# Kernel tuning notes

Measured on AMD Instinct MI355X. Metric: run time of the kernel, lower is better.

## Reference

```python
import jax, jax.numpy as jnp
import numpy as np

B, IMG, P, D, E, S, K, L = 2, 512, 16, 384, 768, 16, 4, 12
G = IMG // P
N = G * G  # 1024 patches

def layer_norm(x, w, b):
    m = x.mean(-1, keepdims=True)
    v = ((x - m) ** 2).mean(-1, keepdims=True)
    return (x - m) / jnp.sqrt(v + 1e-5) * w + b

def silu(x):
    return x * jax.nn.sigmoid(x)

def patch_embed(px, w, b, pos):
    Bz = px.shape[0]
    # non-overlapping patchify == stride-P conv with PxP kernel
    x = px.reshape(Bz, 3, G, P, G, P).transpose(0, 2, 4, 1, 3, 5).reshape(Bz, N, 3 * P * P)
    return x @ w.reshape(D, -1).T + b + pos

def mamba_block(x, norm_w, norm_b, in_w, in_b, conv_w, conv_b, xp_w, xp_b, dt_w, dt_b, A, Dp, out_w, out_b):
    res = x
    x = layer_norm(x, norm_w, norm_b)
    xz = x @ in_w.T + in_b                       # (B,N,2E)
    x_main, z = jnp.split(xz, 2, axis=-1)
    # depthwise causal conv (torch pads K-1 both sides then truncates to N == left pad K-1)
    xc = jax.lax.conv_general_dilated(x_main.transpose(0, 2, 1), conv_w, (1,), [(K - 1, 0)],
                                      dimension_numbers=('NCH', 'OIH', 'NCH'), feature_group_count=E)
    xc = silu((xc + conv_b[:, None]).transpose(0, 2, 1))  # (B,N,E)
    xBC = xc @ xp_w.T + xp_b
    xB, xC = jnp.split(xBC, 2, axis=-1)          # each (B,N,S)
    dt = jnp.clip(jax.nn.softplus(xB @ dt_w.T + dt_b), 1e-4, 1.0)    # (B,N,E)
    dA = jnp.exp(jnp.clip(dt[..., None] * A[None, None], -20.0, 0.0))  # (B,N,E,S)

    def step(h, inp):
        dA_i, xB_i, xC_i, xc_i = inp             # (B,E,S),(B,S),(B,S),(B,E)
        h = dA_i * h + xB_i[:, None, :] * xc_i[:, :, None]
        return h, jnp.einsum('bes,bs->be', h, xC_i)

    h0 = jnp.zeros((x.shape[0], E, S), x.dtype)
    _, ys = jax.lax.scan(step, h0, (dA.transpose(1, 0, 2, 3), xB.transpose(1, 0, 2),
                                    xC.transpose(1, 0, 2), xc.transpose(1, 0, 2)))
    y = ys.transpose(1, 0, 2)                    # (B,N,E)
    y = (y + Dp * xc) * silu(z)
    return res + y @ out_w.T + out_b

def setup_inputs() -> dict:
    key = jax.random.key(0)
    ks = jax.random.split(key, 10)
    rnd = lambda k, shape, s=0.02: jax.random.normal(k, shape, jnp.float32) * s
    return {
        'pixel_values': jax.random.normal(ks[0], (B, 3, IMG, IMG), jnp.float32),
        'patch_w': rnd(ks[1], (D, 3, P, P)),
        'patch_b': jnp.zeros((D,), jnp.float32),
        'pos_embed': rnd(ks[2], (1, N, D)),
        'norm_w': jnp.ones((L, D), jnp.float32), 'norm_b': jnp.zeros((L, D), jnp.float32),
        'in_w': rnd(ks[3], (L, 2 * E, D)), 'in_b': jnp.zeros((L, 2 * E), jnp.float32),
        'conv_w': rnd(ks[4], (L, E, 1, K), 0.3), 'conv_b': jnp.zeros((L, E), jnp.float32),
        'xp_w': rnd(ks[5], (L, 2 * S, E)), 'xp_b': jnp.zeros((L, 2 * S), jnp.float32),
        'dt_w': rnd(ks[6], (L, E, S), 0.1), 'dt_b': jnp.zeros((L, E), jnp.float32),
        'A': -jnp.tile(jnp.arange(1, S + 1, dtype=jnp.float32), (L, E, 1)),
        'Dp': jnp.ones((L, E), jnp.float32),
        'out_w': rnd(ks[7], (L, D, E)), 'out_b': jnp.zeros((L, D), jnp.float32),
        'fnorm_w': jnp.ones((D,), jnp.float32), 'fnorm_b': jnp.zeros((D,), jnp.float32),
        'scale_w': rnd(ks[8], (3, D, D)), 'scale_b': jnp.zeros((3, D), jnp.float32),
    }

def reference(pixel_values, patch_w, patch_b, pos_embed, norm_w, norm_b, in_w, in_b,
              conv_w, conv_b, xp_w, xp_b, dt_w, dt_b, A, Dp, out_w, out_b,
              fnorm_w, fnorm_b, scale_w, scale_b):
    x = patch_embed(pixel_values, patch_w, patch_b, pos_embed)
    layers_per_scale = L // 3
    scales = []
    for i in range(L):
        x = mamba_block(x, norm_w[i], norm_b[i], in_w[i], in_b[i], conv_w[i], conv_b[i],
                        xp_w[i], xp_b[i], dt_w[i], dt_b[i], A[i], Dp[i], out_w[i], out_b[i])
        if i % layers_per_scale == 0 and i // layers_per_scale < 3:
            j = i // layers_per_scale
            scales.append(x @ scale_w[j].T + scale_b[j])
    feats = layer_norm(x, fnorm_w, fnorm_b)
    # stacked: [features, scale_4, scale_8, scale_16] -> (4, B, N, D)
    return jnp.stack([feats] + scales)
```

## Files before the change

### kernel.cpp

```cpp
#include <hip/hip_runtime.h>
#include <hip/hip_bf16.h>

constexpr int Bz = 2, IMG = 512, Pp = 16, D = 384, E = 768, S = 16, L = 12;
constexpr int G = IMG / Pp;
constexpr int Np = G * G;
constexpr int M = Bz * Np;
constexpr int TWO_E = 2 * E;

typedef short bf16x8 __attribute__((ext_vector_type(8)));
typedef float fx4    __attribute__((ext_vector_type(4)));

static __device__ __forceinline__ unsigned short f2bf(float f){
  unsigned int u = __float_as_uint(f);
  u = (u + 0x7FFFu + ((u >> 16) & 1u)) >> 16;
  return (unsigned short)u;
}
static __device__ __forceinline__ float bf2f(unsigned short h){
  return __uint_as_float(((unsigned int)h) << 16);
}

template<int N>
static __device__ __forceinline__ float ror_add(float v){
  int x = __builtin_amdgcn_update_dpp(0, __float_as_int(v), 0x120 | N, 0xF, 0xF, true);
  return v + __int_as_float(x);
}
static __device__ __forceinline__ float row_sum16(float v){
  v = ror_add<8>(v); v = ror_add<4>(v); v = ror_add<2>(v); v = ror_add<1>(v);
  return v;
}

constexpr size_t PW_N = (size_t)D * 768;
constexpr size_t IW_N = (size_t)L * TWO_E * D;
constexpr size_t OW_N = (size_t)L * D * E;
constexpr size_t SW_N = (size_t)3 * D * D;
__device__ short g_pw_h[PW_N], g_pw_l[PW_N];
__device__ short g_iw_h[IW_N], g_iw_l[IW_N];
__device__ short g_ow_h[OW_N], g_ow_l[OW_N];
__device__ short g_swx_h[SW_N], g_swx_l[SW_N];

__global__ void convw_kernel(const float* __restrict__ pw, const float* __restrict__ iw,
                             const float* __restrict__ ow, const float* __restrict__ sw){
  size_t i = (size_t)blockIdx.x * 256 + threadIdx.x;
  if (i >= PW_N + IW_N + OW_N + SW_N) return;
  const float* src; short *dh, *dl; size_t j = i;
  if (j < PW_N){ src = pw; dh = g_pw_h; dl = g_pw_l; }
  else if ((j -= PW_N) < IW_N){ src = iw; dh = g_iw_h; dl = g_iw_l; }
  else if ((j -= IW_N) < OW_N){ src = ow; dh = g_ow_h; dl = g_ow_l; }
  else { j -= OW_N; src = sw; dh = g_swx_h; dl = g_swx_l; }
  float f = src[j];
  unsigned short h = f2bf(f);
  dh[j] = (short)h; dl[j] = (short)f2bf(f - bf2f(h));
}

__global__ void patchify_kernel(const float* __restrict__ px,
                                short* __restrict__ oh, short* __restrict__ ol){
  int idx = blockIdx.x * 256 + threadIdx.x;
  if (idx >= M * 768) return;
  int k = idx % 768, m = idx / 768;
  int b = m / Np, n = m % Np;
  int gy = n / G, gx = n % G;
  int c = k / (Pp * Pp), r = k % (Pp * Pp);
  int py = r / Pp, pxi = r % Pp;
  size_t src = ((size_t)(b * 3 + c) * IMG + gy * Pp + py) * IMG + gx * Pp + pxi;
  float f = px[src];
  unsigned short h = f2bf(f);
  oh[idx] = (short)h; ol[idx] = (short)f2bf(f - bf2f(h));
}

__global__ __launch_bounds__(256)
void layernorm_bf(const float* __restrict__ x, const float* __restrict__ w,
                  const float* __restrict__ bb, short* __restrict__ oh,
                  short* __restrict__ ol){
  int wave = threadIdx.x >> 6, lane = threadIdx.x & 63;
  int row = blockIdx.x * 4 + wave;
  const float* xr = x + (size_t)row * D;
  float v[6], s = 0.f, sq = 0.f;
  #pragma unroll
  for (int i = 0; i < 6; i++){ v[i] = xr[lane + 64 * i]; s += v[i]; sq += v[i] * v[i]; }
  #pragma unroll
  for (int off = 32; off; off >>= 1){ s += __shfl_xor(s, off); sq += __shfl_xor(sq, off); }
  float mean = s * (1.f / D);
  float var  = sq * (1.f / D) - mean * mean;
  float inv  = 1.0f / sqrtf(var + 1e-5f);
  #pragma unroll
  for (int i = 0; i < 6; i++){
    int c = lane + 64 * i;
    float o = (v[i] - mean) * inv * w[c] + bb[c];
    unsigned short h = f2bf(o);
    oh[(size_t)row * D + c] = (short)h;
    ol[(size_t)row * D + c] = (short)f2bf(o - bf2f(h));
  }
}

__global__ __launch_bounds__(256)
void layernorm_f32(const float* __restrict__ x, const float* __restrict__ w,
                   const float* __restrict__ bb, float* __restrict__ outf){
  int wave = threadIdx.x >> 6, lane = threadIdx.x & 63;
  int row = blockIdx.x * 4 + wave;
  const float* xr = x + (size_t)row * D;
  float v[6], s = 0.f, sq = 0.f;
  #pragma unroll
  for (int i = 0; i < 6; i++){ v[i] = xr[lane + 64 * i]; s += v[i]; sq += v[i] * v[i]; }
  #pragma unroll
  for (int off = 32; off; off >>= 1){ s += __shfl_xor(s, off); sq += __shfl_xor(sq, off); }
  float mean = s * (1.f / D);
  float var  = sq * (1.f / D) - mean * mean;
  float inv  = 1.0f / sqrtf(var + 1e-5f);
  #pragma unroll
  for (int i = 0; i < 6; i++){
    int c = lane + 64 * i;
    outf[(size_t)row * D + c] = (v[i] - mean) * inv * w[c] + bb[c];
  }
}

__global__ __launch_bounds__(256)
void gemm_in(const short* __restrict__ Ah, const short* __restrict__ Al,
             size_t woff, const float* __restrict__ bias,
             float* __restrict__ C, float* __restrict__ C2){
  constexpr int BKp = 40;
  __shared__ __align__(16) short sAh[64 * BKp],  sAl[64 * BKp];
  __shared__ __align__(16) short sWh[128 * BKp], sWl[128 * BKp];
  const short* Wh = g_iw_h + woff;
  const short* Wl = g_iw_l + woff;
  const int t = threadIdx.x, wid = t >> 6, lane = t & 63;
  const int m0 = blockIdx.y * 64, n0 = blockIdx.x * 128;
  const int wn = wid * 32;

  fx4 acc[4][2];
  #pragma unroll
  for (int a = 0; a < 4; a++)
    #pragma unroll
    for (int b = 0; b < 2; b++)
      #pragma unroll
      for (int i = 0; i < 4; i++) acc[a][b][i] = 0.f;

  const int rA = t >> 2, kpA = (t & 3) << 3;
  const int rW = t >> 1, kpW = (t & 1) << 4;
  const int row = lane & 15, kq = lane >> 4;

  for (int kt = 0; kt < D; kt += 32){
    *(bf16x8*)&sAh[rA * BKp + kpA] = *(const bf16x8*)(Ah + (size_t)(m0 + rA) * D + kt + kpA);
    *(bf16x8*)&sAl[rA * BKp + kpA] = *(const bf16x8*)(Al + (size_t)(m0 + rA) * D + kt + kpA);
    *(bf16x8*)&sWh[rW * BKp + kpW]     = *(const bf16x8*)(Wh + (size_t)(n0 + rW) * D + kt + kpW);
    *(bf16x8*)&sWh[rW * BKp + kpW + 8] = *(const bf16x8*)(Wh + (size_t)(n0 + rW) * D + kt + kpW + 8);
    *(bf16x8*)&sWl[rW * BKp + kpW]     = *(const bf16x8*)(Wl + (size_t)(n0 + rW) * D + kt + kpW);
    *(bf16x8*)&sWl[rW * BKp + kpW + 8] = *(const bf16x8*)(Wl + (size_t)(n0 + rW) * D + kt + kpW + 8);
    __syncthreads();
    bf16x8 ah[4], al[4], bh[2], bl[2];
    #pragma unroll
    for (int tm = 0; tm < 4; tm++){
      ah[tm] = *(const bf16x8*)&sAh[(tm * 16 + row) * BKp + kq * 8];
      al[tm] = *(const bf16x8*)&sAl[(tm * 16 + row) * BKp + kq * 8];
    }
    #pragma unroll
    for (int tn = 0; tn < 2; tn++){
      bh[tn] = *(const bf16x8*)&sWh[(wn + tn * 16 + row) * BKp + kq * 8];
      bl[tn] = *(const bf16x8*)&sWl[(wn + tn * 16 + row) * BKp + kq * 8];
    }
    #pragma unroll
    for (int tm = 0; tm < 4; tm++)
      #pragma unroll
      for (int tn = 0; tn < 2; tn++){
        acc[tm][tn] = __builtin_amdgcn_mfma_f32_16x16x32_bf16(ah[tm], bh[tn], acc[tm][tn], 0, 0, 0);
        acc[tm][tn] = __builtin_amdgcn_mfma_f32_16x16x32_bf16(ah[tm], bl[tn], acc[tm][tn], 0, 0, 0);
        acc[tm][tn] = __builtin_amdgcn_mfma_f32_16x16x32_bf16(al[tm], bh[tn], acc[tm][tn], 0, 0, 0);
      }
    __syncthreads();
  }

  const int row4 = (lane >> 4) * 4, coln = lane & 15;
  #pragma unroll
  for (int tm = 0; tm < 4; tm++)
    #pragma unroll
    for (int tn = 0; tn < 2; tn++){
      int n = n0 + wn + tn * 16 + coln;
      int mb = m0 + tm * 16 + row4;
      float4 v4;
      float* vp = (float*)&v4;
      #pragma unroll
      for (int i = 0; i < 4; i++) vp[i] = acc[tm][tn][i] + bias[n];
      if (n < E){
        *(float4*)&C[(size_t)n * M + mb] = v4;
      } else {
        #pragma unroll
        for (int i = 0; i < 4; i++){
          float sig = 1.f / (1.f + expf(-vp[i]));
          vp[i] = vp[i] * sig;
        }
        *(float4*)&C2[(size_t)(n - E) * M + mb] = v4;
      }
    }
}

__global__ __launch_bounds__(256)
void gemm_patch(const short* __restrict__ Ah, const short* __restrict__ Al,
                const float* __restrict__ bias, float* __restrict__ C,
                const float* __restrict__ pos){
  constexpr int BKp = 40;
  __shared__ __align__(16) short sAh[64 * BKp], sAl[64 * BKp];
  __shared__ __align__(16) short sWh[64 * BKp], sWl[64 * BKp];
  const int t = threadIdx.x, wid = t >> 6, lane = t & 63;
  const int m0 = blockIdx.y * 64, n0 = blockIdx.x * 64;

  fx4 acc[4];
  #pragma unroll
  for (int a = 0; a < 4; a++)
    #pragma unroll
    for (int i = 0; i < 4; i++) acc[a][i] = 0.f;

  const int r = t >> 2, kp = (t & 3) << 3;
  const int row = lane & 15, kq = lane >> 4;

  for (int kt = 0; kt < 768; kt += 32){
    *(bf16x8*)&sAh[r * BKp + kp] = *(const bf16x8*)(Ah + (size_t)(m0 + r) * 768 + kt + kp);
    *(bf16x8*)&sAl[r * BKp + kp] = *(const bf16x8*)(Al + (size_t)(m0 + r) * 768 + kt + kp);
    *(bf16x8*)&sWh[r * BKp + kp] = *(const bf16x8*)(g_pw_h + (size_t)(n0 + r) * 768 + kt + kp);
    *(bf16x8*)&sWl[r * BKp + kp] = *(const bf16x8*)(g_pw_l + (size_t)(n0 + r) * 768 + kt + kp);
    __syncthreads();
    bf16x8 bh = *(const bf16x8*)&sWh[(wid * 16 + row) * BKp + kq * 8];
    bf16x8 bl = *(const bf16x8*)&sWl[(wid * 16 + row) * BKp + kq * 8];
    #pragma unroll
    for (int tm = 0; tm < 4; tm++){
      bf16x8 ah = *(const bf16x8*)&sAh[(tm * 16 + row) * BKp + kq * 8];
      bf16x8 al = *(const bf16x8*)&sAl[(tm * 16 + row) * BKp + kq * 8];
      acc[tm] = __builtin_amdgcn_mfma_f32_16x16x32_bf16(ah, bh, acc[tm], 0, 0, 0);
      acc[tm] = __builtin_amdgcn_mfma_f32_16x16x32_bf16(ah, bl, acc[tm], 0, 0, 0);
      acc[tm] = __builtin_amdgcn_mfma_f32_16x16x32_bf16(al, bh, acc[tm], 0, 0, 0);
    }
    __syncthreads();
  }

  const int row4 = (lane >> 4) * 4, coln = lane & 15;
  #pragma unroll
  for (int tm = 0; tm < 4; tm++){
    int n = n0 + wid * 16 + coln;
    int mb = m0 + tm * 16 + row4;
    #pragma unroll
    for (int i = 0; i < 4; i++){
      int m = mb + i;
      C[(size_t)m * D + n] = acc[tm][i] + bias[n] + pos[(size_t)(m & (Np - 1)) * D + n];
    }
  }
}

__global__ __launch_bounds__(256)
void gemm_scale(const float* __restrict__ A, size_t woff,
                const float* __restrict__ bias, float* __restrict__ C){
  constexpr int BKp = 40;
  __shared__ __align__(16) short sAh[64 * BKp], sAl[64 * BKp];
  __shared__ __align__(16) short sWh[64 * BKp], sWl[64 * BKp];
  const short* Wh = g_swx_h + woff;
  const short* Wl = g_swx_l + woff;
  const int t = threadIdx.x, wid = t >> 6, lane = t & 63;
  const int m0 = blockIdx.y * 64, n0 = blockIdx.x * 64;

  fx4 acc[4];
  #pragma unroll
  for (int a = 0; a < 4; a++)
    #pragma unroll
    for (int i = 0; i < 4; i++) acc[a][i] = 0.f;

  const int r = t >> 2, kp = (t & 3) << 3;
  const int row = lane & 15, kq = lane >> 4;

  for (int kt = 0; kt < D; kt += 32){
    {
      const float* ap = A + (size_t)(m0 + r) * D + kt + kp;
      float4 f0 = *(const float4*)ap, f1 = *(const float4*)(ap + 4);
      float f[8] = {f0.x, f0.y, f0.z, f0.w, f1.x, f1.y, f1.z, f1.w};
      short hh[8], ll[8];
      #pragma unroll
      for (int i = 0; i < 8; i++){
        unsigned short h = f2bf(f[i]);
        hh[i] = (short)h; ll[i] = (short)f2bf(f[i] - bf2f(h));
      }
      *(bf16x8*)&sAh[r * BKp + kp] = *(bf16x8*)hh;
      *(bf16x8*)&sAl[r * BKp + kp] = *(bf16x8*)ll;
    }
    *(bf16x8*)&sWh[r * BKp + kp] = *(const bf16x8*)(Wh + (size_t)(n0 + r) * D + kt + kp);
    *(bf16x8*)&sWl[r * BKp + kp] = *(const bf16x8*)(Wl + (size_t)(n0 + r) * D + kt + kp);
    __syncthreads();
    bf16x8 bh = *(const bf16x8*)&sWh[(wid * 16 + row) * BKp + kq * 8];
    bf16x8 bl = *(const bf16x8*)&sWl[(wid * 16 + row) * BKp + kq * 8];
    #pragma unroll
    for (int tm = 0; tm < 4; tm++){
      bf16x8 ah = *(const bf16x8*)&sAh[(tm * 16 + row) * BKp + kq * 8];
      bf16x8 al = *(const bf16x8*)&sAl[(tm * 16 + row) * BKp + kq * 8];
      acc[tm] = __builtin_amdgcn_mfma_f32_16x16x32_bf16(ah, bh, acc[tm], 0, 0, 0);
      acc[tm] = __builtin_amdgcn_mfma_f32_16x16x32_bf16(ah, bl, acc[tm], 0, 0, 0);
      acc[tm] = __builtin_amdgcn_mfma_f32_16x16x32_bf16(al, bh, acc[tm], 0, 0, 0);
    }
    __syncthreads();
  }

  const int row4 = (lane >> 4) * 4, coln = lane & 15;
  #pragma unroll
  for (int tm = 0; tm < 4; tm++){
    int n = n0 + wid * 16 + coln;
    int mb = m0 + tm * 16 + row4;
    #pragma unroll
    for (int i = 0; i < 4; i++){
      int m = mb + i;
      C[(size_t)m * D + n] = acc[tm][i] + bias[n];
    }
  }
}

__global__ __launch_bounds__(256)
void gemm_bf_at(const short* __restrict__ ATh, const short* __restrict__ ATl, int K,
                size_t woff, const float* __restrict__ bias,
                float* __restrict__ C, int ncols, float* __restrict__ zbuf){
  constexpr int BKp = 40;
  __shared__ __align__(16) short sAh[64 * BKp], sAl[64 * BKp];
  __shared__ __align__(16) short sWh[64 * BKp], sWl[64 * BKp];
  const short* Wh = g_ow_h + woff;
  const short* Wl = g_ow_l + woff;
  const int t = threadIdx.x, wid = t >> 6, lane = t & 63;
  const int m0 = blockIdx.y * 64, n0 = blockIdx.x * 64;

  fx4 acc[4];
  #pragma unroll
  for (int a = 0; a < 4; a++)
    #pragma unroll
    for (int i = 0; i < 4; i++) acc[a][i] = 0.f;

  const int rw = t >> 2, kpw = (t & 3) << 3;
  const int kr2 = (t & 15) * 2, mc4 = (t >> 4) * 4;
  const int row = lane & 15, kq = lane >> 4;

  for (int kt = 0; kt < K; kt += 32){
    {
      const uint2 h0 = *(const uint2*)(ATh + (size_t)(kt + kr2) * M + m0 + mc4);
      const uint2 h1 = *(const uint2*)(ATh + (size_t)(kt + kr2 + 1) * M + m0 + mc4);
      const uint2 l0 = *(const uint2*)(ATl + (size_t)(kt + kr2) * M + m0 + mc4);
      const uint2 l1 = *(const uint2*)(ATl + (size_t)(kt + kr2 + 1) * M + m0 + mc4);
      const unsigned int h0a[2] = {h0.x, h0.y}, h1a[2] = {h1.x, h1.y};
      const unsigned int l0a[2] = {l0.x, l0.y}, l1a[2] = {l1.x, l1.y};
      #pragma unroll
      for (int j = 0; j < 4; j++){
        unsigned int s0 = (h0a[j >> 1] >> ((j & 1) * 16)) & 0xFFFFu;
        unsigned int s1 = (h1a[j >> 1] >> ((j & 1) * 16)) & 0xFFFFu;
        *(unsigned int*)&sAh[(mc4 + j) * BKp + kr2] = s0 | (s1 << 16);
        unsigned int t0 = (l0a[j >> 1] >> ((j & 1) * 16)) & 0xFFFFu;
        unsigned int t1 = (l1a[j >> 1] >> ((j & 1) * 16)) & 0xFFFFu;
        *(unsigned int*)&sAl[(mc4 + j) * BKp + kr2] = t0 | (t1 << 16);
      }
    }
    *(bf16x8*)&sWh[rw * BKp + kpw] = *(const bf16x8*)(Wh + (size_t)(n0 + rw) * K + kt + kpw);
    *(bf16x8*)&sWl[rw * BKp + kpw] = *(const bf16x8*)(Wl + (size_t)(n0 + rw) * K + kt + kpw);
    __syncthreads();
    bf16x8 bh = *(const bf16x8*)&sWh[(wid * 16 + row) * BKp + kq * 8];
    bf16x8 bl = *(const bf16x8*)&sWl[(wid * 16 + row) * BKp + kq * 8];
    #pragma unroll
    for (int tm = 0; tm < 4; tm++){
      bf16x8 ah = *(const bf16x8*)&sAh[(tm * 16 + row) * BKp + kq * 8];
      bf16x8 al = *(const bf16x8*)&sAl[(tm * 16 + row) * BKp + kq * 8];
      acc[tm] = __builtin_amdgcn_mfma_f32_16x16x32_bf16(ah, bh, acc[tm], 0, 0, 0);
      acc[tm] = __builtin_amdgcn_mfma_f32_16x16x32_bf16(ah, bl, acc[tm], 0, 0, 0);
      acc[tm] = __builtin_amdgcn_mfma_f32_16x16x32_bf16(al, bh, acc[tm], 0, 0, 0);
    }
    __syncthreads();
  }

  const int row4 = (lane >> 4) * 4, coln = lane & 15;
  #pragma unroll
  for (int tm = 0; tm < 4; tm++)
    #pragma unroll
    for (int i = 0; i < 4; i++){
      int m = m0 + tm * 16 + row4 + i;
      int n = n0 + wid * 16 + coln;
      float v = acc[tm][i] + bias[n] + C[(size_t)m * ncols + n];
      C[(size_t)m * ncols + n] = v;
    }

  int gid = blockIdx.y * gridDim.x + blockIdx.x;
  int idx = gid * 256 + t;
  if (idx < M * 16)
    *(float2*)&zbuf[idx * 2] = make_float2(0.f, 0.f);
}

__global__ __launch_bounds__(256)
void gemm_xp(const float* __restrict__ xcT, const float* __restrict__ W,
             const float* __restrict__ bias, float* __restrict__ C){
  __shared__ float As[16][64 + 1];
  __shared__ float Ws[16][32 + 1];
  int tid = threadIdx.x;
  int tx = tid & 15, ty = tid >> 4;
  int m0 = blockIdx.y * 64, kb = blockIdx.x * 192;
  float acc[4][2];
  #pragma unroll
  for (int i = 0; i < 4; i++){ acc[i][0] = 0.f; acc[i][1] = 0.f; }
  for (int kt = kb; kt < kb + 192; kt += 16){
    #pragma unroll
    for (int ps = 0; ps < 4; ps++){
      int rr = (tid >> 6) + 4 * ps, mc = tid & 63;
      As[rr][mc] = xcT[(size_t)(kt + rr) * M + m0 + mc];
    }
    if (tid < 128){
      int c = tid >> 2, kk = (tid & 3) << 2;
      const float* wp = W + (size_t)c * E + kt + kk;
      Ws[kk + 0][c] = wp[0]; Ws[kk + 1][c] = wp[1];
      Ws[kk + 2][c] = wp[2]; Ws[kk + 3][c] = wp[3];
    }
    __syncthreads();
    #pragma unroll
    for (int k = 0; k < 16; k++){
      float a[4], w[2];
      #pragma unroll
      for (int i = 0; i < 4; i++) a[i] = As[k][ty * 4 + i];
      w[0] = Ws[k][tx * 2]; w[1] = Ws[k][tx * 2 + 1];
      #pragma unroll
      for (int i = 0; i < 4; i++){ acc[i][0] += a[i] * w[0]; acc[i][1] += a[i] * w[1]; }
    }
    __syncthreads();
  }
  #pragma unroll
  for (int i = 0; i < 4; i++){
    int m = m0 + ty * 4 + i;
    #pragma unroll
    for (int j = 0; j < 2; j++){
      int n = tx * 2 + j;
      float v = acc[i][j];
      if (blockIdx.x == 0) v += bias[n];
      atomicAdd(&C[(size_t)m * 32 + n], v);
    }
  }
}

__global__ __launch_bounds__(256)
void conv_silu_t(const float* __restrict__ xmT, const float* __restrict__ cw,
                 const float* __restrict__ cb, float* __restrict__ xcT){
  const int e = blockIdx.x, t = threadIdx.x;
  const float w0 = cw[e * 4], w1 = cw[e * 4 + 1], w2 = cw[e * 4 + 2], w3 = cw[e * 4 + 3];
  const float bias = cb[e];
  const float* src = xmT + (size_t)e * M;
  float* dst = xcT + (size_t)e * M;
  int mb = t * 8;
  #pragma unroll
  for (int j = 0; j < 8; j++){
    int m = mb + j, n = m & (Np - 1);
    float acc = bias + w3 * src[m];
    if (n >= 1) acc += w2 * src[m - 1];
    if (n >= 2) acc += w1 * src[m - 2];
    if (n >= 3) acc += w0 * src[m - 3];
    float sig = 1.f / (1.f + expf(-acc));
    dst[m] = acc * sig;
  }
}

__global__ __launch_bounds__(256)
void scan_kernel(const float* __restrict__ xcT, const float* __restrict__ zst,
                 const float* __restrict__ xBC,
                 const float* __restrict__ Aptr, const float* __restrict__ Dp,
                 const float* __restrict__ dt_w, const float* __restrict__ dt_b,
                 short* __restrict__ yh, short* __restrict__ yl){
  __shared__ float yloc[16 * 65];
  __shared__ float sdx[64 * 34];
  __shared__ float hloc[16][16], prodA[16][16], Hin[16][16];
  const int t = threadIdx.x, g = t >> 4, s = t & 15;
  const int r = blockIdx.x, b = r / E, e = r % E;
  const float a   = Aptr[e * S + s];
  const float dpe = Dp[e];
  const float* xcp = xcT + (size_t)e * M + b * Np;
  const float* zsp = zst + (size_t)e * M + b * Np;
  const int bNp = b * Np;

  {
    const float* dw = dt_w + e * 16;
    float4 w0 = *(const float4*)dw,       w1 = *(const float4*)(dw + 4);
    float4 w2 = *(const float4*)(dw + 8), w3 = *(const float4*)(dw + 12);
    float db = dt_b[e];
    for (int q = t; q < 1024; q += 256){
      const float* xb = xBC + (size_t)(bNp + q) * 32;
      float4 a0 = *(const float4*)xb,       a1 = *(const float4*)(xb + 4);
      float4 a2 = *(const float4*)(xb + 8), a3 = *(const float4*)(xb + 12);
      float v = db + a0.x * w0.x + a0.y * w0.y + a0.z * w0.z + a0.w * w0.w
                   + a1.x * w1.x + a1.y * w1.y + a1.z * w1.z + a1.w * w1.w
                   + a2.x * w2.x + a2.y * w2.y + a2.z * w2.z + a2.w * w2.w
                   + a3.x * w3.x + a3.y * w3.y + a3.z * w3.z + a3.w * w3.w;
      v = (v > 15.f) ? v : log1pf(expf(v));
      v = fminf(fmaxf(v, 1e-4f), 1.0f);
      *(float2*)&sdx[(q & 63) * 34 + (q >> 6) * 2] = make_float2(v, xcp[q]);
    }
  }
  __syncthreads();

  const int n0 = g * 64;
  const int mbase = bNp + n0;

  float h = 0.f, Pa = 1.f;
  #pragma unroll 8
  for (int i = 0; i < 64; i++){
    float2 dx = *(const float2*)&sdx[i * 34 + g * 2];
    float xb = xBC[(size_t)(mbase + i) * 32 + s];
    float dA = __expf(dx.x * a);
    h = dA * h + xb * dx.y;
    Pa *= dA;
  }
  hloc[g][s] = h; prodA[g][s] = Pa;
  __syncthreads();

  if (t < 16){
    float H = 0.f;
    #pragma unroll
    for (int g2 = 0; g2 < 16; g2++){
      Hin[g2][t] = H;
      H = prodA[g2][t] * H + hloc[g2][t];
    }
  }
  __syncthreads();

  h = Hin[g][s];
  #pragma unroll 8
  for (int i = 0; i < 64; i++){
    float2 dx = *(const float2*)&sdx[i * 34 + g * 2];
    int m = mbase + i;
    float xb  = xBC[(size_t)m * 32 + s];
    float xcs = xBC[(size_t)m * 32 + 16 + s];
    float dA = __expf(dx.x * a);
    h = dA * h + xb * dx.y;
    float p = row_sum16(h * xcs);
    if (s == 0) yloc[g * 65 + i] = p + dpe * dx.y;
  }
  __syncthreads();

  {
    int n4 = t * 4;
    float4 z4 = *(const float4*)&zsp[n4];
    const float* zp = (const float*)&z4;
    int gy = n4 >> 6, iy = n4 & 63;
    unsigned int hpack[2], lpack[2];
    #pragma unroll
    for (int half = 0; half < 2; half++){
      unsigned int hp = 0, lp = 0;
      #pragma unroll
      for (int j = 0; j < 2; j++){
        float val = yloc[gy * 65 + iy + half * 2 + j] * zp[half * 2 + j];
        unsigned short hh = f2bf(val);
        unsigned short ll = f2bf(val - bf2f(hh));
        hp |= ((unsigned int)hh) << (16 * j);
        lp |= ((unsigned int)ll) << (16 * j);
      }
      hpack[half] = hp; lpack[half] = lp;
    }
    size_t o = (size_t)e * M + bNp + n4;
    *(uint2*)&yh[o] = make_uint2(hpack[0], hpack[1]);
    *(uint2*)&yl[o] = make_uint2(lpack[0], lpack[1]);
  }
}

extern "C" void kernel_launch(void* const* d_in, const int* in_sizes, int n_in,
                              void* d_out, int out_size, void* d_ws, size_t ws_size,
                              hipStream_t stream){
  const float* px      = (const float*)d_in[0];
  const float* patch_w = (const float*)d_in[1];
  const float* patch_b = (const float*)d_in[2];
  const float* pos     = (const float*)d_in[3];
  const float* norm_w  = (const float*)d_in[4];
  const float* norm_b  = (const float*)d_in[5];
  const float* in_w    = (const float*)d_in[6];
  const float* in_b    = (const float*)d_in[7];
  const float* conv_w  = (const float*)d_in[8];
  const float* conv_b  = (const float*)d_in[9];
  const float* xp_w    = (const float*)d_in[10];
  const float* xp_b    = (const float*)d_in[11];
  const float* dt_w    = (const float*)d_in[12];
  const float* dt_b    = (const float*)d_in[13];
  const float* Aab     = (const float*)d_in[14];
  const float* Dp      = (const float*)d_in[15];
  const float* out_w   = (const float*)d_in[16];
  const float* out_b   = (const float*)d_in[17];
  const float* fnorm_w = (const float*)d_in[18];
  const float* fnorm_b = (const float*)d_in[19];
  const float* scale_w = (const float*)d_in[20];
  const float* scale_b = (const float*)d_in[21];
  float* out = (float*)d_out;

  float* x   = (float*)d_ws;
  float* xmT = x + (size_t)M * D;
  float* zst = xmT + (size_t)M * E;
  float* xcT = zst + (size_t)M * E;
  float* xBC = xcT + (size_t)M * E;
  short* xnh = (short*)(xBC + (size_t)M * 32);
  short* xnl = xnh + (size_t)M * D;
  short* yh  = (short*)xmT;
  short* yl  = yh + (size_t)M * E;
  short* pbh = yh, *pbl = yl;

  constexpr size_t TOTW = PW_N + IW_N + OW_N + SW_N;
  convw_kernel<<<(int)((TOTW + 255) / 256), 256, 0, stream>>>(patch_w, in_w, out_w, scale_w);
  hipMemsetAsync(xBC, 0, (size_t)M * 32 * sizeof(float), stream);

  patchify_kernel<<<(M * 768 + 255) / 256, 256, 0, stream>>>(px, pbh, pbl);
  gemm_patch<<<dim3(D / 64, M / 64), 256, 0, stream>>>(pbh, pbl, patch_b, x, pos);

  for (int l = 0; l < L; l++){
    layernorm_bf<<<M / 4, 256, 0, stream>>>(x, norm_w + l * D, norm_b + l * D, xnh, xnl);
    gemm_in<<<dim3(TWO_E / 128, M / 64), 256, 0, stream>>>(
        xnh, xnl, (size_t)l * TWO_E * D, in_b + l * TWO_E, xmT, zst);
    conv_silu_t<<<E, 256, 0, stream>>>(
        xmT, conv_w + (size_t)l * E * 4, conv_b + l * E, xcT);
    gemm_xp<<<dim3(4, M / 64), 256, 0, stream>>>(
        xcT, xp_w + (size_t)l * 32 * E, xp_b + l * 32, xBC);
    scan_kernel<<<Bz * E, 256, 0, stream>>>(
        xcT, zst, xBC, Aab + (size_t)l * E * S, Dp + l * E,
        dt_w + (size_t)l * E * S, dt_b + l * E, yh, yl);
    gemm_bf_at<<<dim3(D / 64, M / 64), 256, 0, stream>>>(
        yh, yl, E, (size_t)l * D * E, out_b + l * D, x, D, xBC);
    if (l % 4 == 0 && l / 4 < 3){
      int j = l / 4;
      gemm_scale<<<dim3(D / 64, M / 64), 256, 0, stream>>>(
          x, (size_t)j * D * D, scale_b + j * D, out + (size_t)(1 + j) * M * D);
    }
  }
  layernorm_f32<<<M / 4, 256, 0, stream>>>(x, fnorm_w, fnorm_b, out);
}
```

Measured before the change: 1.617 ms.

## Restructure selective scan into 64 chunks with 4 states per thread

The per-channel scan kernel now splits the 1024-step sequence into 64 chunks of 16 positions. Each thread holds 4 of the 16 states in registers, replacing 16 chunks of 64 steps with one state per thread. Chunk decay products come from a single exp2 of the summed dt, the exponentials use raw v_exp_f32 with pre-scaled A, and the output reduction becomes a 4-lane DPP quad sum instead of a 16-lane row sum. The goal is a shorter serial dependency chain, vectorized float4 loads of B and C, and less exp work. In exchange, the serial cross-chunk carry loop run by 16 threads grows from 16 to 64 steps, and the D-skip term moves to the epilogue.

```diff
diff --git a/kernel.cpp b/kernel.cpp
--- a/kernel.cpp
+++ b/kernel.cpp
@@ -19,13 +19,17 @@
   return __uint_as_float(((unsigned int)h) << 16);
 }
 
-template<int N>
-static __device__ __forceinline__ float ror_add(float v){
-  int x = __builtin_amdgcn_update_dpp(0, __float_as_int(v), 0x120 | N, 0xF, 0xF, true);
-  return v + __int_as_float(x);
-}
-static __device__ __forceinline__ float row_sum16(float v){
-  v = ror_add<8>(v); v = ror_add<4>(v); v = ror_add<2>(v); v = ror_add<1>(v);
+static __device__ __forceinline__ float fexp2(float x){
+  float r;
+  asm("v_exp_f32 %0, %1" : "=v"(r) : "v"(x));
+  return r;
+}
+
+static __device__ __forceinline__ float quad_sum(float v){
+  int a = __builtin_amdgcn_update_dpp(0, __float_as_int(v), 0xB1, 0xF, 0xF, true);
+  v += __int_as_float(a);
+  int b = __builtin_amdgcn_update_dpp(0, __float_as_int(v), 0x4E, 0xF, 0xF, true);
+  v += __int_as_float(b);
   return v;
 }
 
@@ -454,23 +458,29 @@
                  const float* __restrict__ Aptr, const float* __restrict__ Dp,
                  const float* __restrict__ dt_w, const float* __restrict__ dt_b,
                  short* __restrict__ yh, short* __restrict__ yl){
-  __shared__ float yloc[16 * 65];
-  __shared__ float sdx[64 * 34];
-  __shared__ float hloc[16][16], prodA[16][16], Hin[16][16];
-  const int t = threadIdx.x, g = t >> 4, s = t & 15;
+  __shared__ float sdx[2176];
+  __shared__ float sHin[64 * 16];
+  __shared__ float scr[2048];
+  const int t = threadIdx.x;
+  const int c = t >> 2;
+  const int u = t & 3;
   const int r = blockIdx.x, b = r / E, e = r % E;
-  const float a   = Aptr[e * S + s];
+  const int bNp = b * Np;
   const float dpe = Dp[e];
-  const float* xcp = xcT + (size_t)e * M + b * Np;
-  const float* zsp = zst + (size_t)e * M + b * Np;
-  const int bNp = b * Np;
+  constexpr float LOG2E = 1.4426950408889634f;
+  float4 a4 = *(const float4*)(Aptr + e * S + u * 4);
+  const float a20 = a4.x * LOG2E, a21 = a4.y * LOG2E, a22 = a4.z * LOG2E, a23 = a4.w * LOG2E;
+  const float* xcp = xcT + (size_t)e * M + bNp;
+  const float* zsp = zst + (size_t)e * M + bNp;
 
   {
     const float* dw = dt_w + e * 16;
     float4 w0 = *(const float4*)dw,       w1 = *(const float4*)(dw + 4);
     float4 w2 = *(const float4*)(dw + 8), w3 = *(const float4*)(dw + 12);
     float db = dt_b[e];
-    for (int q = t; q < 1024; q += 256){
+    #pragma unroll
+    for (int p = 0; p < 4; p++){
+      int q = t + p * 256;
       const float* xb = xBC + (size_t)(bNp + q) * 32;
       float4 a0 = *(const float4*)xb,       a1 = *(const float4*)(xb + 4);
       float4 a2 = *(const float4*)(xb + 8), a3 = *(const float4*)(xb + 12);
@@ -480,47 +490,70 @@
                    + a3.x * w3.x + a3.y * w3.y + a3.z * w3.z + a3.w * w3.w;
       v = (v > 15.f) ? v : log1pf(expf(v));
       v = fminf(fmaxf(v, 1e-4f), 1.0f);
-      *(float2*)&sdx[(q & 63) * 34 + (q >> 6) * 2] = make_float2(v, xcp[q]);
+      int w = (q << 1) + ((q >> 4) << 1);
+      *(float2*)&sdx[w] = make_float2(v, xcp[q]);
     }
   }
   __syncthreads();
 
-  const int n0 = g * 64;
-  const int mbase = bNp + n0;
-
-  float h = 0.f, Pa = 1.f;
-  #pragma unroll 8
-  for (int i = 0; i < 64; i++){
-    float2 dx = *(const float2*)&sdx[i * 34 + g * 2];
-    float xb = xBC[(size_t)(mbase + i) * 32 + s];
-    float dA = __expf(dx.x * a);
-    h = dA * h + xb * dx.y;
-    Pa *= dA;
-  }
-  hloc[g][s] = h; prodA[g][s] = Pa;
+  const int pos0 = c * 16;
+  const int wbase = (pos0 << 1) + ((pos0 >> 4) << 1);
+  const float* xbp  = xBC + ((size_t)(bNp + pos0) * 32 + u * 4);
+  const float* xcsp = xbp + 16;
+
+  float h0 = 0.f, h1 = 0.f, h2 = 0.f, h3 = 0.f, sdt = 0.f;
+  #pragma unroll
+  for (int i = 0; i < 16; i++){
+    float2 dx = *(const float2*)&sdx[wbase + 2 * i];
+    float4 xb = *(const float4*)(xbp + (size_t)i * 32);
+    float dt = dx.x, xcv = dx.y;
+    sdt += dt;
+    float e0 = fexp2(dt * a20), e1 = fexp2(dt * a21);
+    float e2 = fexp2(dt * a22), e3 = fexp2(dt * a23);
+    h0 = e0 * h0 + xb.x * xcv;
+    h1 = e1 * h1 + xb.y * xcv;
+    h2 = e2 * h2 + xb.z * xcv;
+    h3 = e3 * h3 + xb.w * xcv;
+  }
+  {
+    float p0 = fexp2(sdt * a20), p1 = fexp2(sdt * a21);
+    float p2 = fexp2(sdt * a22), p3 = fexp2(sdt * a23);
+    *(float4*)&scr[c * 16 + u * 4]        = make_float4(h0, h1, h2, h3);
+    *(float4*)&scr[1024 + c * 16 + u * 4] = make_float4(p0, p1, p2, p3);
+  }
   __syncthreads();
 
   if (t < 16){
     float H = 0.f;
-    #pragma unroll
-    for (int g2 = 0; g2 < 16; g2++){
-      Hin[g2][t] = H;
-      H = prodA[g2][t] * H + hloc[g2][t];
+    #pragma unroll 8
+    for (int cc = 0; cc < 64; cc++){
+      sHin[cc * 16 + t] = H;
+      H = scr[1024 + cc * 16 + t] * H + scr[cc * 16 + t];
     }
   }
   __syncthreads();
 
-  h = Hin[g][s];
-  #pragma unroll 8
-  for (int i = 0; i < 64; i++){
-    float2 dx = *(const float2*)&sdx[i * 34 + g * 2];
-    int m = mbase + i;
-    float xb  = xBC[(size_t)m * 32 + s];
-    float xcs = xBC[(size_t)m * 32 + 16 + s];
-    float dA = __expf(dx.x * a);
-    h = dA * h + xb * dx.y;
-    float p = row_sum16(h * xcs);
-    if (s == 0) yloc[g * 65 + i] = p + dpe * dx.y;
+  {
+    float4 hin = *(const float4*)&sHin[c * 16 + u * 4];
+    h0 = hin.x; h1 = hin.y; h2 = hin.z; h3 = hin.w;
+  }
+  float* yloc = scr;
+  const int ybase = pos0 + ((pos0 >> 4) << 2);
+  #pragma unroll
+  for (int i = 0; i < 16; i++){
+    float2 dx = *(const float2*)&sdx[wbase + 2 * i];
+    float4 xb  = *(const float4*)(xbp  + (size_t)i * 32);
+    float4 xcs = *(const float4*)(xcsp + (size_t)i * 32);
+    float dt = dx.x, xcv = dx.y;
+    float e0 = fexp2(dt * a20), e1 = fexp2(dt * a21);
+    float e2 = fexp2(dt * a22), e3 = fexp2(dt * a23);
+    h0 = e0 * h0 + xb.x * xcv;
+    h1 = e1 * h1 + xb.y * xcv;
+    h2 = e2 * h2 + xb.z * xcv;
+    h3 = e3 * h3 + xb.w * xcv;
+    float yp = h0 * xcs.x + h1 * xcs.y + h2 * xcs.z + h3 * xcs.w;
+    yp = quad_sum(yp);
+    if (u == 0) yloc[ybase + i] = yp;
   }
   __syncthreads();
 
@@ -528,14 +561,17 @@
     int n4 = t * 4;
     float4 z4 = *(const float4*)&zsp[n4];
     const float* zp = (const float*)&z4;
-    int gy = n4 >> 6, iy = n4 & 63;
+    int yb = n4 + ((n4 >> 4) << 2);
+    int xw = (n4 << 1) + ((n4 >> 4) << 1);
     unsigned int hpack[2], lpack[2];
     #pragma unroll
     for (int half = 0; half < 2; half++){
       unsigned int hp = 0, lp = 0;
       #pragma unroll
       for (int j = 0; j < 2; j++){
-        float val = yloc[gy * 65 + iy + half * 2 + j] * zp[half * 2 + j];
+        int jj = half * 2 + j;
+        float xcv = sdx[xw + 2 * jj + 1];
+        float val = (yloc[yb + jj] + dpe * xcv) * zp[jj];
         unsigned short hh = f2bf(val);
         unsigned short ll = f2bf(val - bf2f(hh));
         hp |= ((unsigned int)hh) << (16 * j);
```

Result: faster. 1.555 ms (-3.8%).
